# Optimization experiments

Measured on AMD Instinct MI355X. Metric: run time of the kernel, lower is better.

## Reference

```python
import jax, jax.numpy as jnp
import numpy as np

B, S, H, D = 4, 2048, 16, 64
DM = H * D  # 1024


def setup_inputs() -> dict:
    key = jax.random.key(0)
    ks = jax.random.split(key, 10)
    scale = 1.0 / np.sqrt(DM)
    return {
        "input_q": jax.random.normal(ks[0], (B, S, DM), jnp.float32),
        "input_k": jax.random.normal(ks[1], (B, S, DM), jnp.float32),
        "input_v": jax.random.normal(ks[2], (B, S, DM), jnp.float32),
        "mask": jax.random.uniform(ks[3], (B, 1, S, S), jnp.float32),
        "Wq": jax.random.normal(ks[4], (DM, DM), jnp.float32) * scale,
        "bq": jnp.zeros((DM,), jnp.float32),
        "Wk": jax.random.normal(ks[5], (DM, DM), jnp.float32) * scale,
        "bk": jnp.zeros((DM,), jnp.float32),
        "Wv": jax.random.normal(ks[6], (DM, DM), jnp.float32) * scale,
        "bv": jnp.zeros((DM,), jnp.float32),
    }


def _split_heads(x):
    # [B, S, H*D] -> [B, H, S, D]
    b, s, _ = x.shape
    return x.reshape(b, s, H, D).transpose(0, 2, 1, 3)


def reference(input_q, input_k, input_v, mask, Wq, bq, Wk, bk, Wv, bv):
    q = _split_heads(input_q @ Wq + bq)
    k = _split_heads(input_k @ Wk + bk)
    v = _split_heads(input_v @ Wv + bv)
    # scores: [B, H, Sq, Sk]
    qk = jnp.einsum("bhqd,bhkd->bhqk", q, k) / jnp.sqrt(jnp.float32(D))
    qk = qk + mask * (-1e9)
    # NOTE: original code applies softmax over axis=0 (batch axis) — preserved faithfully.
    value_weights = jax.nn.softmax(qk, axis=0)
    value = jnp.einsum("bhqk,bhkd->bhqd", value_weights, v)
    # [B, H, S, D] -> [B, S, H*D]; final self.dense is a plain keras Layer (identity).
    value = value.transpose(0, 2, 1, 3).reshape(B, S, DM)
    return value
```

## Files before the change

kernel.cpp:

```cpp
#include <hip/hip_runtime.h>
#include <stdint.h>

#define B_  4
#define S_  2048
#define H_  16
#define DH_ 64
#define DM_ 1024

typedef __attribute__((ext_vector_type(8))) short bf16x8;
typedef __attribute__((ext_vector_type(4))) short bf16x4;
typedef __attribute__((ext_vector_type(4))) float f32x4;

__device__ __forceinline__ ushort f2bf(float x){
  uint32_t u = __float_as_uint(x);
  u += 0x7FFFu + ((u >> 16) & 1u);
  return (ushort)(u >> 16);
}
__device__ __forceinline__ uint32_t pack2(float a, float b){
  return (uint32_t)f2bf(a) | ((uint32_t)f2bf(b) << 16);
}
__device__ __forceinline__ uint32_t packtr(float a, float b){
  return __builtin_amdgcn_perm(__float_as_uint(b), __float_as_uint(a), 0x07060302u);
}
__device__ __forceinline__ f32x4 zero4(){ f32x4 z; z.x=0.f;z.y=0.f;z.z=0.f;z.w=0.f; return z; }

__device__ __forceinline__ void async16(void* lds, const void* g){
  __builtin_amdgcn_global_load_lds(
      (const __attribute__((address_space(1))) unsigned int*)g,
      (__attribute__((address_space(3))) unsigned int*)lds, 16, 0, 0);
}

__device__ __forceinline__ float exp2_hw(float x){
#if __has_builtin(__builtin_amdgcn_exp2f)
  return __builtin_amdgcn_exp2f(x);
#else
  float r; asm("v_exp_f32 %0, %1" : "=v"(r) : "v"(x)); return r;
#endif
}

__device__ __forceinline__ f32x4 mfma16(bf16x4 a, bf16x4 b, f32x4 c){
#if __has_builtin(__builtin_amdgcn_mfma_f32_16x16x16bf16_1k)
  return __builtin_amdgcn_mfma_f32_16x16x16bf16_1k(a, b, c, 0, 0, 0);
#elif __has_builtin(__builtin_amdgcn_mfma_f32_16x16x16_bf16)
  return __builtin_amdgcn_mfma_f32_16x16x16_bf16(a, b, c, 0, 0, 0);
#else
  f32x4 d = c;
  asm("v_mfma_f32_16x16x16_bf16 %0, %1, %2, %0" : "+v"(d) : "v"(a), "v"(b));
  return d;
#endif
}

__global__ __launch_bounds__(256) void conv2(const float* __restrict__ a,
                                             const float* __restrict__ b,
                                             ushort* __restrict__ oa,
                                             ushort* __restrict__ ob){
  const float* src = (blockIdx.y==0) ? a : b;
  ushort* dst      = (blockIdx.y==0) ? oa : ob;
  size_t i = ((size_t)blockIdx.x*256 + threadIdx.x)*8;
  float4 x0 = *(const float4*)&src[i];
  float4 x1 = *(const float4*)&src[i+4];
  uint4 p;
  p.x = pack2(x0.x,x0.y); p.y = pack2(x0.z,x0.w);
  p.z = pack2(x1.x,x1.y); p.w = pack2(x1.z,x1.w);
  *(uint4*)&dst[i] = p;
}

__global__ __launch_bounds__(256) void wtrans3(const float* __restrict__ Wq,
                                               const float* __restrict__ Wk,
                                               const float* __restrict__ Wv,
                                               ushort* __restrict__ Tq,
                                               ushort* __restrict__ Tk,
                                               ushort* __restrict__ Tv){
  const float* W = (blockIdx.z==0) ? Wq : (blockIdx.z==1) ? Wk : Wv;
  ushort* Wt     = (blockIdx.z==0) ? Tq : (blockIdx.z==1) ? Tk : Tv;
  __shared__ __align__(16) float t[32][33];
  int n0 = blockIdx.x * 32, k0 = blockIdx.y * 32;
  int col = threadIdx.x & 31, rg = threadIdx.x >> 5;
  #pragma unroll
  for (int i = 0; i < 4; i++){
    int r = rg + i*8;
    t[r][col] = W[(size_t)(k0 + r) * DM_ + n0 + col];
  }
  __syncthreads();
  #pragma unroll
  for (int i = 0; i < 4; i++){
    int r = rg + i*8;
    Wt[(size_t)(n0 + r) * DM_ + k0 + col] = f2bf(t[col][r]);
  }
}

__global__ __launch_bounds__(256, 4) void gemm_qk(
    const ushort* __restrict__ Xq, const ushort* __restrict__ Xk,
    const ushort* __restrict__ Wtq, const ushort* __restrict__ Wtk,
    const float* __restrict__ bq, const float* __restrict__ bk,
    ushort* __restrict__ Qo, ushort* __restrict__ Ko)
{
  const ushort* Xb = (blockIdx.z==0) ? Xq : Xk;
  const ushort* Wt = (blockIdx.z==0) ? Wtq : Wtk;
  const float* bias = (blockIdx.z==0) ? bq : bk;
  ushort* out = (blockIdx.z==0) ? Qo : Ko;

  __shared__ __align__(16) ushort lw[128*64];
  __shared__ __align__(16) ushort lx[128*64];
  int tid = threadIdx.x;
  int l = tid & 63, w = tid >> 6;
  int ln = l & 15, lq = l >> 4;
  int sbase = blockIdx.x * 128;
  int fbase = blockIdx.y * 128;
  int wm = w >> 1, wn = w & 1;

  f32x4 acc[4][4];
  #pragma unroll
  for (int i=0;i<4;i++)
    #pragma unroll
    for(int j=0;j<4;j++) acc[i][j] = zero4();

  for (int k0 = 0; k0 < DM_; k0 += 64){
    #pragma unroll
    for (int i = 0; i < 4; i++){
      int inst = w*4 + i;
      int chunk = inst*64 + l;
      int row = chunk >> 3, slot = chunk & 7;
      int kc = slot ^ (row & 7);
      async16((char*)lw + inst*1024, &Wt[(size_t)(fbase+row)*DM_ + k0 + kc*8]);
      async16((char*)lx + inst*1024, &Xb[(size_t)(sbase+row)*DM_ + k0 + kc*8]);
    }
    __syncthreads();
    #pragma unroll
    for (int ks=0; ks<2; ks++){
      bf16x8 af[4], bfr[4];
      #pragma unroll
      for (int i=0;i<4;i++){
        int ar = wm*64 + i*16 + ln;
        int g = ks*4 + lq;
        af[i] = *(const bf16x8*)&lw[ar*64 + (g ^ (ar&7))*8];
      }
      #pragma unroll
      for (int j=0;j<4;j++){
        int br = wn*64 + j*16 + ln;
        int g = ks*4 + lq;
        bfr[j] = *(const bf16x8*)&lx[br*64 + (g ^ (br&7))*8];
      }
      #pragma unroll
      for (int i=0;i<4;i++)
        #pragma unroll
        for (int j=0;j<4;j++)
          acc[i][j] = __builtin_amdgcn_mfma_f32_16x16x32_bf16(af[i], bfr[j], acc[i][j], 0,0,0);
    }
    __syncthreads();
  }
  #pragma unroll
  for (int i=0;i<4;i++){
    int fr = fbase + wm*64 + i*16 + (lq<<2);
    float4 bv = *(const float4*)&bias[fr];
    int h = fr >> 6, d0 = fr & 63;
    #pragma unroll
    for (int j=0;j<4;j++){
      int s = sbase + wn*64 + j*16 + ln;
      int b = s >> 11, sq = s & 2047;
      f32x4 v = acc[i][j];
      uint2 pk;
      pk.x = pack2(v.x + bv.x, v.y + bv.y);
      pk.y = pack2(v.z + bv.z, v.w + bv.w);
      *(uint2*)&out[(((size_t)(b*H_ + h))*S_ + sq)*DH_ + d0] = pk;
    }
  }
}

__global__ __launch_bounds__(256, 2) void gemm_v(
    const float* __restrict__ X, const ushort* __restrict__ Wt,
    const float* __restrict__ bias, ushort* __restrict__ out)
{
  __shared__ __align__(16) ushort lw[128*64];
  __shared__ __align__(16) ushort lx[128*64];
  int tid = threadIdx.x;
  int l = tid & 63, w = tid >> 6;
  int ln = l & 15, lq = l >> 4;
  int sbase = blockIdx.x * 128;
  int fbase = blockIdx.y * 128;
  int wm = w >> 1, wn = w & 1;

  f32x4 acc[4][4];
  #pragma unroll
  for (int i=0;i<4;i++)
    #pragma unroll
    for(int j=0;j<4;j++) acc[i][j] = zero4();

  for (int k0 = 0; k0 < DM_; k0 += 64){
    #pragma unroll
    for (int i = 0; i < 4; i++){
      int inst = w*4 + i;
      int chunk = inst*64 + l;
      int row = chunk >> 3, slot = chunk & 7;
      int kc = slot ^ (row & 7);
      async16((char*)lw + inst*1024, &Wt[(size_t)(fbase+row)*DM_ + k0 + kc*8]);
    }
    #pragma unroll
    for (int r = 0; r < 4; r++){
      int flat = r*256 + tid;
      int row = flat >> 3, c = flat & 7;
      int g = c ^ (row & 7);
      const float* xs = &X[(size_t)(sbase+row)*DM_ + k0 + g*8];
      float4 x0 = *(const float4*)xs;
      float4 x1 = *(const float4*)(xs+4);
      uint4 p;
      p.x = pack2(x0.x, x0.y); p.y = pack2(x0.z, x0.w);
      p.z = pack2(x1.x, x1.y); p.w = pack2(x1.z, x1.w);
      *(uint4*)&lx[row*64 + c*8] = p;
    }
    __syncthreads();
    #pragma unroll
    for (int ks=0; ks<2; ks++){
      bf16x8 af[4], bfr[4];
      #pragma unroll
      for (int i=0;i<4;i++){
        int ar = wm*64 + i*16 + ln;
        int g = ks*4 + lq;
        af[i] = *(const bf16x8*)&lx[ar*64 + (g ^ (ar&7))*8];
      }
      #pragma unroll
      for (int j=0;j<4;j++){
        int br = wn*64 + j*16 + ln;
        int g = ks*4 + lq;
        bfr[j] = *(const bf16x8*)&lw[br*64 + (g ^ (br&7))*8];
      }
      #pragma unroll
      for (int i=0;i<4;i++)
        #pragma unroll
        for (int j=0;j<4;j++)
          acc[i][j] = __builtin_amdgcn_mfma_f32_16x16x32_bf16(af[i], bfr[j], acc[i][j], 0,0,0);
    }
    __syncthreads();
  }
  #pragma unroll
  for (int j=0;j<4;j++){
    int fc = fbase + wn*64 + j*16 + ln;
    float bv = bias[fc];
    int h = fc >> 6, d = fc & 63;
    #pragma unroll
    for (int i=0;i<4;i++){
      int s = sbase + wm*64 + i*16 + (lq<<2);
      int b = s >> 11, sq = s & 2047;
      f32x4 v = acc[i][j];
      uint2 pk;
      pk.x = pack2(v.x + bv, v.y + bv);
      pk.y = pack2(v.z + bv, v.w + bv);
      *(uint2*)&out[(((size_t)(b*H_ + h))*DH_ + d)*S_ + sq] = pk;
    }
  }
}

#define CS_LOG2 0.18033688011112042f
#define CM_LOG2 -1.4426950408889634e9f

__global__ __launch_bounds__(256, 2) void attn(
    const ushort* __restrict__ Q, const ushort* __restrict__ K,
    const ushort* __restrict__ Vt, const float* __restrict__ mask,
    float* __restrict__ out)
{
  __shared__ __align__(16) ushort Kl[2][4096];
  __shared__ __align__(16) ushort Vl[2][4096];

  const int tid = threadIdx.x;
  const int l = tid & 63, w = tid >> 6;
  const int ln = l & 15, lq = l >> 4;
  const int bid = blockIdx.x;
  const int h = bid & 15, qtg = bid >> 4;
  const int q0 = (qtg*4 + w)*16;

  const ushort* Kroot = K  + (size_t)h*S_*DH_;
  const ushort* Vroot = Vt + (size_t)h*DH_*S_;

  uint ksrc[2], vsrc[2];
  int kdst[2], vdst[2];
  #pragma unroll
  for (int j=0;j<2;j++){
    int inst = w*2 + j;
    int cc = inst*64 + l;
    { int b = cc>>7, r = (cc>>3)&15, c = cc&7;
      ksrc[j] = (uint)(b*(H_*S_*DH_) + r*DH_ + (c ^ (r&7))*8);
      kdst[j] = inst*512; }
    { int b = cc>>7, rem = cc&127, r = rem>>1, c = rem&1;
      vsrc[j] = (uint)(b*(H_*DH_*S_) + r*S_ + c*8);
      vdst[j] = inst*512; }
  }

  bf16x8 qf[4][2];
  #pragma unroll
  for (int b=0;b<4;b++){
    const ushort* Qb = Q + (((size_t)(b*H_ + h))*S_ + q0 + ln)*DH_;
    #pragma unroll
    for (int ks=0;ks<2;ks++)
      qf[b][ks] = *(const bf16x8*)&Qb[ks*32 + lq*8];
  }

  f32x4 of[4][4];
  #pragma unroll
  for (int b=0;b<4;b++)
    #pragma unroll
    for (int dt=0;dt<4;dt++) of[b][dt] = zero4();

  const uint moff = (uint)((q0 + ln)*S_ + lq*4);

  #pragma unroll
  for (int j=0;j<2;j++){
    async16(&Kl[0][kdst[j]], Kroot + ksrc[j]);
    async16(&Vl[0][vdst[j]], Vroot + vsrc[j]);
  }
  __builtin_amdgcn_sched_barrier(0);
  f32x4 mk[4];
  #pragma unroll
  for (int b=0;b<4;b++)
    mk[b] = *(const f32x4*)&mask[(size_t)b*S_*S_ + moff];
  asm volatile("s_waitcnt vmcnt(4)\n\ts_barrier" ::: "memory");

#define ATTN_ITER(CUR, KKV)                                                     \
  {                                                                             \
    const int kk_ = (KKV);                                                      \
    const int kn_ = (kk_ + 16) & (S_ - 1);                                      \
       \
    _Pragma("unroll")                                                           \
    for (int j=0;j<2;j++){                                                      \
      async16(&Kl[(CUR)^1][kdst[j]], Kroot + ksrc[j] + (uint)kn_*DH_);          \
      async16(&Vl[(CUR)^1][vdst[j]], Vroot + vsrc[j] + (uint)kn_);              \
    }                                                                           \
    __builtin_amdgcn_sched_barrier(0);                                          \
                                             \
    bf16x8 kf[4][2];                                                            \
    _Pragma("unroll")                                                           \
    for (int b=0;b<4;b++)                                                       \
      _Pragma("unroll")                                                         \
      for (int ks=0;ks<2;ks++)                                                  \
        kf[b][ks] = *(const bf16x8*)&Kl[CUR][b*1024 + ln*64 + ((ks*4+lq) ^ (ln&7))*8]; \
    bf16x4 vf[4][4];                                                            \
    _Pragma("unroll")                                                           \
    for (int b=0;b<4;b++)                                                       \
      _Pragma("unroll")                                                         \
      for (int dt=0;dt<4;dt++)                                                  \
        vf[b][dt] = *(const bf16x4*)&Vl[CUR][b*1024 + (dt*16+ln)*16 + lq*4];    \
             \
    f32x4 sacc[4];                                                              \
    __builtin_amdgcn_s_setprio(1);                                              \
    _Pragma("unroll")                                                           \
    for (int b=0;b<4;b++){                                                      \
      f32x4 a_ = __builtin_amdgcn_mfma_f32_16x16x32_bf16(kf[b][0], qf[b][0], zero4(), 0,0,0); \
      sacc[b]  = __builtin_amdgcn_mfma_f32_16x16x32_bf16(kf[b][1], qf[b][1], a_, 0,0,0); \
    }                                                                           \
    __builtin_amdgcn_s_setprio(0);                                              \
                            \
    float pw[4][4];                                                             \
    _Pragma("unroll")                                                           \
    for (int j=0;j<4;j++){                                                      \
      float s0 = __builtin_fmaf(sacc[0][j], CS_LOG2, mk[0][j]*CM_LOG2);         \
      float s1 = __builtin_fmaf(sacc[1][j], CS_LOG2, mk[1][j]*CM_LOG2);         \
      float s2 = __builtin_fmaf(sacc[2][j], CS_LOG2, mk[2][j]*CM_LOG2);         \
      float s3 = __builtin_fmaf(sacc[3][j], CS_LOG2, mk[3][j]*CM_LOG2);         \
      float mx = fmaxf(fmaxf(s0,s1), fmaxf(s2,s3));                             \
      float e0 = exp2_hw(s0-mx), e1 = exp2_hw(s1-mx);                           \
      float e2 = exp2_hw(s2-mx), e3 = exp2_hw(s3-mx);                           \
      float inv = __builtin_amdgcn_rcpf((e0+e1)+(e2+e3));                       \
      pw[0][j]=e0*inv; pw[1][j]=e1*inv; pw[2][j]=e2*inv; pw[3][j]=e3*inv;       \
    }                                                                           \
     \
    _Pragma("unroll")                                                           \
    for (int b=0;b<4;b++)                                                       \
      mk[b] = *(const f32x4*)&mask[(size_t)b*S_*S_ + moff + (uint)kn_];         \
                \
    bf16x4 pf[4];                                                               \
    _Pragma("unroll")                                                           \
    for (int b=0;b<4;b++){                                                      \
      uint2 up;                                                                 \
      up.x = packtr(pw[b][0], pw[b][1]);                                        \
      up.y = packtr(pw[b][2], pw[b][3]);                                        \
      pf[b] = __builtin_bit_cast(bf16x4, up);                                   \
    }                                                                           \
                                                          \
    __builtin_amdgcn_s_setprio(1);                                              \
    _Pragma("unroll")                                                           \
    for (int b=0;b<4;b++)                                                       \
      _Pragma("unroll")                                                         \
      for (int dt=0;dt<4;dt++)                                                  \
        of[b][dt] = mfma16(vf[b][dt], pf[b], of[b][dt]);                        \
    __builtin_amdgcn_s_setprio(0);                                              \
             \
    asm volatile("s_waitcnt vmcnt(4)\n\ts_barrier" ::: "memory");               \
  }

  #pragma unroll 1
  for (int kk = 0; kk < S_; kk += 32){
    ATTN_ITER(0, kk);
    ATTN_ITER(1, kk+16);
  }
#undef ATTN_ITER

  #pragma unroll
  for (int b=0;b<4;b++){
    float* ob = out + ((size_t)b*S_ + q0 + ln)*DM_ + h*DH_;
    #pragma unroll
    for (int dt=0;dt<4;dt++)
      *(f32x4*)&ob[dt*16 + lq*4] = of[b][dt];
  }
}

extern "C" void kernel_launch(void* const* d_in, const int* in_sizes, int n_in,
                              void* d_out, int out_size, void* d_ws, size_t ws_size,
                              hipStream_t stream)
{
  const float* xq   = (const float*)d_in[0];
  const float* xk   = (const float*)d_in[1];
  const float* xv   = (const float*)d_in[2];
  const float* mask = (const float*)d_in[3];
  const float* Wq   = (const float*)d_in[4];
  const float* bq   = (const float*)d_in[5];
  const float* Wk   = (const float*)d_in[6];
  const float* bk   = (const float*)d_in[7];
  const float* Wv   = (const float*)d_in[8];
  const float* bv   = (const float*)d_in[9];
  float* out = (float*)d_out;

  char* ws = (char*)d_ws;
  ushort* Wtq = (ushort*)(ws);
  ushort* Wtk = (ushort*)(ws + (2ull<<20));
  ushort* Wtv = (ushort*)(ws + (4ull<<20));
  ushort* Xbq = (ushort*)(ws + (6ull<<20));
  ushort* Xbk = (ushort*)(ws + (22ull<<20));
  ushort* Qb  = (ushort*)(ws + (38ull<<20));
  ushort* Kb  = (ushort*)(ws + (54ull<<20));
  ushort* Vtb = Xbq;

  conv2<<<dim3(4096,2), 256, 0, stream>>>(xq, xk, Xbq, Xbk);
  wtrans3<<<dim3(32,32,3), 256, 0, stream>>>(Wq, Wk, Wv, Wtq, Wtk, Wtv);

  gemm_qk<<<dim3(64,8,2), 256, 0, stream>>>(Xbq, Xbk, Wtq, Wtk, bq, bk, Qb, Kb);
  gemm_v<<<dim3(64,8), 256, 0, stream>>>(xv, Wtv, bv, Vtb);

  attn<<<512, 256, 0, stream>>>(Qb, Kb, Vtb, mask, out);
}
```

Measured before the change: 476.8 us.

## Double attention key tile to 32 and use 16x16x32 MFMA for PV

Each pipeline stage now covers 32 keys instead of 16, so K/V LDS buffers double and there are half as many barrier and async-load rounds. K and V are staged in a new swizzled layout. The PV product switches from 16x16x16 MFMAs with bf16x4 operands to 16x16x32 MFMAs with bf16x8 operands, packing two 16-key probability tiles into one fragment. This raises LDS use and register pressure (double mask registers), which may reduce occupancy under launch_bounds(256,2).

Result: faster. 452.2 us (-5.2%).

```diff
diff --git a/kernel.cpp b/kernel.cpp
--- a/kernel.cpp
+++ b/kernel.cpp
@@ -8,7 +8,6 @@
 #define DM_ 1024
 
 typedef __attribute__((ext_vector_type(8))) short bf16x8;
-typedef __attribute__((ext_vector_type(4))) short bf16x4;
 typedef __attribute__((ext_vector_type(4))) float f32x4;
 
 __device__ __forceinline__ ushort f2bf(float x){
@@ -35,18 +34,6 @@
   return __builtin_amdgcn_exp2f(x);
 #else
   float r; asm("v_exp_f32 %0, %1" : "=v"(r) : "v"(x)); return r;
-#endif
-}
-
-__device__ __forceinline__ f32x4 mfma16(bf16x4 a, bf16x4 b, f32x4 c){
-#if __has_builtin(__builtin_amdgcn_mfma_f32_16x16x16bf16_1k)
-  return __builtin_amdgcn_mfma_f32_16x16x16bf16_1k(a, b, c, 0, 0, 0);
-#elif __has_builtin(__builtin_amdgcn_mfma_f32_16x16x16_bf16)
-  return __builtin_amdgcn_mfma_f32_16x16x16_bf16(a, b, c, 0, 0, 0);
-#else
-  f32x4 d = c;
-  asm("v_mfma_f32_16x16x16_bf16 %0, %1, %2, %0" : "+v"(d) : "v"(a), "v"(b));
-  return d;
 #endif
 }
 
@@ -258,8 +245,8 @@
     const ushort* __restrict__ Vt, const float* __restrict__ mask,
     float* __restrict__ out)
 {
-  __shared__ __align__(16) ushort Kl[2][4096];
-  __shared__ __align__(16) ushort Vl[2][4096];
+  __shared__ __align__(16) ushort Kl[2][8192];
+  __shared__ __align__(16) ushort Vl[2][8192];
 
   const int tid = threadIdx.x;
   const int l = tid & 63, w = tid >> 6;
@@ -271,18 +258,26 @@
   const ushort* Kroot = K  + (size_t)h*S_*DH_;
   const ushort* Vroot = Vt + (size_t)h*DH_*S_;
 
-  uint ksrc[2], vsrc[2];
-  int kdst[2], vdst[2];
-  #pragma unroll
-  for (int j=0;j<2;j++){
-    int inst = w*2 + j;
-    int cc = inst*64 + l;
-    { int b = cc>>7, r = (cc>>3)&15, c = cc&7;
-      ksrc[j] = (uint)(b*(H_*S_*DH_) + r*DH_ + (c ^ (r&7))*8);
-      kdst[j] = inst*512; }
-    { int b = cc>>7, rem = cc&127, r = rem>>1, c = rem&1;
-      vsrc[j] = (uint)(b*(H_*DH_*S_) + r*S_ + c*8);
-      vdst[j] = inst*512; }
+  uint ksrc[4], vsrc[4];
+  int kdst[4], vdst[4];
+  #pragma unroll
+  for (int j=0;j<4;j++){
+    int ck = (w*4 + j)*64 + l;
+    {
+      int t = ck >> 9, rem = ck & 511, b = rem >> 7, rr = rem & 127;
+      int x = rr >> 3, cs = rr & 7;
+      int c = cs ^ (x & 7);
+      int krow = (x >> 2)*8 + t*4 + (x & 3);
+      ksrc[j] = (uint)(b*(H_*S_*DH_) + krow*DH_ + c*8);
+      kdst[j] = ck*16;
+    }
+    {
+      int b = ck >> 8, rem = ck & 255, r = rem >> 3, ss = rem & 7;
+      int s = ss ^ (r & 7);
+      int d = r + (s >> 2)*32, kc = s & 3;
+      vsrc[j] = (uint)(b*(H_*DH_*S_) + d*S_ + kc*8);
+      vdst[j] = ck*16;
+    }
   }
 
   bf16x8 qf[4][2];
@@ -300,96 +295,100 @@
     #pragma unroll
     for (int dt=0;dt<4;dt++) of[b][dt] = zero4();
 
-  const uint moff = (uint)((q0 + ln)*S_ + lq*4);
-
-  #pragma unroll
-  for (int j=0;j<2;j++){
-    async16(&Kl[0][kdst[j]], Kroot + ksrc[j]);
-    async16(&Vl[0][vdst[j]], Vroot + vsrc[j]);
-  }
+  const float* mrow = mask + (size_t)(q0 + ln)*S_ + lq*8;
+
+  #pragma unroll
+  for (int j=0;j<4;j++) async16((char*)Kl[0] + kdst[j], Kroot + ksrc[j]);
+  #pragma unroll
+  for (int j=0;j<4;j++) async16((char*)Vl[0] + vdst[j], Vroot + vsrc[j]);
   __builtin_amdgcn_sched_barrier(0);
-  f32x4 mk[4];
-  #pragma unroll
-  for (int b=0;b<4;b++)
-    mk[b] = *(const f32x4*)&mask[(size_t)b*S_*S_ + moff];
-  asm volatile("s_waitcnt vmcnt(4)\n\ts_barrier" ::: "memory");
+  f32x4 mk[2][4];
+  #pragma unroll
+  for (int t=0;t<2;t++)
+    #pragma unroll
+    for (int b=0;b<4;b++)
+      mk[t][b] = *(const f32x4*)&mrow[(size_t)b*S_*S_ + t*4];
+  asm volatile("s_waitcnt vmcnt(8)\n\ts_barrier" ::: "memory");
 
 #define ATTN_ITER(CUR, KKV)                                                     \
   {                                                                             \
     const int kk_ = (KKV);                                                      \
-    const int kn_ = (kk_ + 16) & (S_ - 1);                                      \
-       \
+    const int kn_ = (kk_ + 32) & (S_ - 1);                                      \
+           \
     _Pragma("unroll")                                                           \
-    for (int j=0;j<2;j++){                                                      \
-      async16(&Kl[(CUR)^1][kdst[j]], Kroot + ksrc[j] + (uint)kn_*DH_);          \
-      async16(&Vl[(CUR)^1][vdst[j]], Vroot + vsrc[j] + (uint)kn_);              \
+    for (int j=0;j<4;j++)                                                       \
+      async16((char*)Kl[(CUR)^1] + kdst[j], Kroot + ksrc[j] + (uint)kn_*DH_);   \
+    _Pragma("unroll")                                                           \
+    for (int j=0;j<4;j++)                                                       \
+      async16((char*)Vl[(CUR)^1] + vdst[j], Vroot + vsrc[j] + (uint)kn_);       \
+    __builtin_amdgcn_sched_barrier(0);                                          \
+                                         \
+    uint2 up[2][4];                                                             \
+    _Pragma("unroll")                                                           \
+    for (int t_=0;t_<2;t_++){                                                   \
+      bf16x8 kf[4][2];                                                          \
+      _Pragma("unroll")                                                         \
+      for (int b=0;b<4;b++)                                                     \
+        _Pragma("unroll")                                                       \
+        for (int ks=0;ks<2;ks++)                                                \
+          kf[b][ks] = *(const bf16x8*)&Kl[CUR][((t_*4+b)*16 + ln)*64 + (((ks*4+lq) ^ (ln&7)))*8]; \
+      f32x4 sacc[4];                                                            \
+      __builtin_amdgcn_s_setprio(1);                                            \
+      _Pragma("unroll")                                                         \
+      for (int b=0;b<4;b++){                                                    \
+        f32x4 a_ = __builtin_amdgcn_mfma_f32_16x16x32_bf16(kf[b][0], qf[b][0], zero4(), 0,0,0); \
+        sacc[b]  = __builtin_amdgcn_mfma_f32_16x16x32_bf16(kf[b][1], qf[b][1], a_, 0,0,0);      \
+      }                                                                         \
+      __builtin_amdgcn_s_setprio(0);                                            \
+      float pw[4][4];                                                           \
+      _Pragma("unroll")                                                         \
+      for (int j=0;j<4;j++){                                                    \
+        float s0 = __builtin_fmaf(sacc[0][j], CS_LOG2, mk[t_][0][j]*CM_LOG2);   \
+        float s1 = __builtin_fmaf(sacc[1][j], CS_LOG2, mk[t_][1][j]*CM_LOG2);   \
+        float s2 = __builtin_fmaf(sacc[2][j], CS_LOG2, mk[t_][2][j]*CM_LOG2);   \
+        float s3 = __builtin_fmaf(sacc[3][j], CS_LOG2, mk[t_][3][j]*CM_LOG2);   \
+        float mx = fmaxf(fmaxf(s0,s1), fmaxf(s2,s3));                           \
+        float e0 = exp2_hw(s0-mx), e1 = exp2_hw(s1-mx);                         \
+        float e2 = exp2_hw(s2-mx), e3 = exp2_hw(s3-mx);                         \
+        float inv = __builtin_amdgcn_rcpf((e0+e1)+(e2+e3));                     \
+        pw[0][j]=e0*inv; pw[1][j]=e1*inv; pw[2][j]=e2*inv; pw[3][j]=e3*inv;     \
+      }                                                                         \
+      _Pragma("unroll")                                                         \
+      for (int b=0;b<4;b++){                                                    \
+        up[t_][b].x = packtr(pw[b][0], pw[b][1]);                               \
+        up[t_][b].y = packtr(pw[b][2], pw[b][3]);                               \
+      }                                                                         \
     }                                                                           \
-    __builtin_amdgcn_sched_barrier(0);                                          \
-                                             \
-    bf16x8 kf[4][2];                                                            \
+                                               \
     _Pragma("unroll")                                                           \
-    for (int b=0;b<4;b++)                                                       \
-      _Pragma("unroll")                                                         \
-      for (int ks=0;ks<2;ks++)                                                  \
-        kf[b][ks] = *(const bf16x8*)&Kl[CUR][b*1024 + ln*64 + ((ks*4+lq) ^ (ln&7))*8]; \
-    bf16x4 vf[4][4];                                                            \
-    _Pragma("unroll")                                                           \
-    for (int b=0;b<4;b++)                                                       \
-      _Pragma("unroll")                                                         \
-      for (int dt=0;dt<4;dt++)                                                  \
-        vf[b][dt] = *(const bf16x4*)&Vl[CUR][b*1024 + (dt*16+ln)*16 + lq*4];    \
-             \
-    f32x4 sacc[4];                                                              \
-    __builtin_amdgcn_s_setprio(1);                                              \
+    for (int t_=0;t_<2;t_++)                                                    \
+      _Pragma("unroll")                                                         \
+      for (int b=0;b<4;b++)                                                     \
+        mk[t_][b] = *(const f32x4*)&mrow[(size_t)b*S_*S_ + kn_ + t_*4];         \
+                   \
     _Pragma("unroll")                                                           \
     for (int b=0;b<4;b++){                                                      \
-      f32x4 a_ = __builtin_amdgcn_mfma_f32_16x16x32_bf16(kf[b][0], qf[b][0], zero4(), 0,0,0); \
-      sacc[b]  = __builtin_amdgcn_mfma_f32_16x16x32_bf16(kf[b][1], qf[b][1], a_, 0,0,0); \
+      uint4 u4; u4.x = up[0][b].x; u4.y = up[0][b].y;                           \
+      u4.z = up[1][b].x; u4.w = up[1][b].y;                                     \
+      bf16x8 pf = __builtin_bit_cast(bf16x8, u4);                               \
+      bf16x8 vf[4];                                                             \
+      _Pragma("unroll")                                                         \
+      for (int dt=0;dt<4;dt++)                                                  \
+        vf[dt] = *(const bf16x8*)&Vl[CUR][(b*32 + (dt&1)*16 + ln)*64 + ((((dt>>1)*4 + lq) ^ (ln&7)))*8]; \
+      __builtin_amdgcn_s_setprio(1);                                            \
+      _Pragma("unroll")                                                         \
+      for (int dt=0;dt<4;dt++)                                                  \
+        of[b][dt] = __builtin_amdgcn_mfma_f32_16x16x32_bf16(vf[dt], pf, of[b][dt], 0,0,0); \
+      __builtin_amdgcn_s_setprio(0);                                            \
     }                                                                           \
-    __builtin_amdgcn_s_setprio(0);                                              \
-                            \
-    float pw[4][4];                                                             \
-    _Pragma("unroll")                                                           \
-    for (int j=0;j<4;j++){                                                      \
-      float s0 = __builtin_fmaf(sacc[0][j], CS_LOG2, mk[0][j]*CM_LOG2);         \
-      float s1 = __builtin_fmaf(sacc[1][j], CS_LOG2, mk[1][j]*CM_LOG2);         \
-      float s2 = __builtin_fmaf(sacc[2][j], CS_LOG2, mk[2][j]*CM_LOG2);         \
-      float s3 = __builtin_fmaf(sacc[3][j], CS_LOG2, mk[3][j]*CM_LOG2);         \
-      float mx = fmaxf(fmaxf(s0,s1), fmaxf(s2,s3));                             \
-      float e0 = exp2_hw(s0-mx), e1 = exp2_hw(s1-mx);                           \
-      float e2 = exp2_hw(s2-mx), e3 = exp2_hw(s3-mx);                           \
-      float inv = __builtin_amdgcn_rcpf((e0+e1)+(e2+e3));                       \
-      pw[0][j]=e0*inv; pw[1][j]=e1*inv; pw[2][j]=e2*inv; pw[3][j]=e3*inv;       \
-    }                                                                           \
-     \
-    _Pragma("unroll")                                                           \
-    for (int b=0;b<4;b++)                                                       \
-      mk[b] = *(const f32x4*)&mask[(size_t)b*S_*S_ + moff + (uint)kn_];         \
-                \
-    bf16x4 pf[4];                                                               \
-    _Pragma("unroll")                                                           \
-    for (int b=0;b<4;b++){                                                      \
-      uint2 up;                                                                 \
-      up.x = packtr(pw[b][0], pw[b][1]);                                        \
-      up.y = packtr(pw[b][2], pw[b][3]);                                        \
-      pf[b] = __builtin_bit_cast(bf16x4, up);                                   \
-    }                                                                           \
-                                                          \
-    __builtin_amdgcn_s_setprio(1);                                              \
-    _Pragma("unroll")                                                           \
-    for (int b=0;b<4;b++)                                                       \
-      _Pragma("unroll")                                                         \
-      for (int dt=0;dt<4;dt++)                                                  \
-        of[b][dt] = mfma16(vf[b][dt], pf[b], of[b][dt]);                        \
-    __builtin_amdgcn_s_setprio(0);                                              \
-             \
-    asm volatile("s_waitcnt vmcnt(4)\n\ts_barrier" ::: "memory");               \
+                  \
+    asm volatile("s_waitcnt vmcnt(8)\n\ts_barrier" ::: "memory");               \
   }
 
   #pragma unroll 1
-  for (int kk = 0; kk < S_; kk += 32){
+  for (int kk = 0; kk < S_; kk += 64){
     ATTN_ITER(0, kk);
-    ATTN_ITER(1, kk+16);
+    ATTN_ITER(1, kk+32);
   }
 #undef ATTN_ITER
 
```
